# Kernel optimization log

Measured on AMD Instinct MI355X. Metric: run time of the kernel, lower is better.

## Reference

```python
import jax, jax.numpy as jnp
import numpy as np

D_MODEL = 1024
NUM_HEADS = 16
HEAD_DIM = D_MODEL // NUM_HEADS
B, SX, SKV = 4, 2048, 2048


def setup_inputs() -> dict:
    key = jax.random.key(0)
    ks = jax.random.split(key, 6)
    scale = 1.0 / np.sqrt(D_MODEL)
    x = jax.random.normal(ks[0], (B, SX, D_MODEL), dtype=jnp.float32)
    kv = jax.random.normal(ks[1], (B, SKV, D_MODEL), dtype=jnp.float32)
    Wq = jax.random.normal(ks[2], (D_MODEL, D_MODEL), dtype=jnp.float32) * scale
    Wk = jax.random.normal(ks[3], (D_MODEL, D_MODEL), dtype=jnp.float32) * scale
    Wv = jax.random.normal(ks[4], (D_MODEL, D_MODEL), dtype=jnp.float32) * scale
    Wo = jax.random.normal(ks[5], (D_MODEL, D_MODEL), dtype=jnp.float32) * scale
    # causal mask: positions where mask == 0 are filled with -inf
    mask = jnp.tril(jnp.ones((SX, SKV), dtype=jnp.int32))[None, None, :, :]
    return {"x": x, "kv": kv, "mask": mask, "Wq": Wq, "Wk": Wk, "Wv": Wv, "Wo": Wo}


def reference(x, kv, mask, Wq, Wk, Wv, Wo):
    # nn.Linear(bias=False): y = x @ W.T
    q = jnp.einsum('bsd,ed->bse', x, Wq)
    k = jnp.einsum('bsd,ed->bse', kv, Wk)
    v = jnp.einsum('bsd,ed->bse', kv, Wv)
    # split heads -> (B, H, S, hd)
    q = q.reshape(B, SX, NUM_HEADS, HEAD_DIM).transpose(0, 2, 1, 3)
    k = k.reshape(B, SKV, NUM_HEADS, HEAD_DIM).transpose(0, 2, 1, 3)
    v = v.reshape(B, SKV, NUM_HEADS, HEAD_DIM).transpose(0, 2, 1, 3)
    scores = jnp.einsum('bhqd,bhkd->bhqk', q, k) / jnp.sqrt(
        jnp.asarray(HEAD_DIM, dtype=q.dtype))
    scores = jnp.where(mask == 0, -jnp.inf, scores)
    attn = jax.nn.softmax(scores, axis=-1)  # dropout p=0.0 -> identity
    context = jnp.einsum('bhqk,bhkd->bhqd', attn, v)
    context = context.transpose(0, 2, 1, 3).reshape(B, SX, D_MODEL)
    return jnp.einsum('bsd,ed->bse', context, Wo)
```

## Files before the change

### kernel.cpp

```cpp
#include <hip/hip_runtime.h>
#include <hip/hip_bf16.h>
#include <math.h>

#define DM   1024
#define SEQ  2048
#define NH   16
#define HD   64
#define BATCH 4

#define QSCALE 0.180336879f

typedef __attribute__((ext_vector_type(8))) short bf16x8;
typedef __attribute__((ext_vector_type(4))) short short4v;
typedef __attribute__((ext_vector_type(4))) float f32x4;
typedef __attribute__((ext_vector_type(4))) float float4v;

#define S_VMCNT(n) asm volatile("s_waitcnt vmcnt(" #n ")" ::: "memory")

static __device__ inline short f2bf(float f) {
  union { float f; unsigned u; } v; v.f = f;
  unsigned u = v.u + 0x7fff + ((v.u >> 16) & 1);
  return (short)(u >> 16);
}

static __device__ __forceinline__ void async16(const void* g, void* l) {
  __builtin_amdgcn_global_load_lds(
      (const __attribute__((address_space(1))) void*)g,
      (__attribute__((address_space(3))) void*)l, 16, 0, 0);
}

__global__ void conv_all(const float* __restrict__ x, const float* __restrict__ kv,
                         const float* __restrict__ Wq, const float* __restrict__ Wk,
                         const float* __restrict__ Wv, const float* __restrict__ Wo,
                         short* __restrict__ xh, short* __restrict__ kvh,
                         short* __restrict__ Wqh, short* __restrict__ Wkh,
                         short* __restrict__ Wvh, short* __restrict__ Woh)
{
  const int blk = blockIdx.x;
  const float* src; short* hi; int base;
  if (blk < 8192)       { src = x;  hi = xh;  base = blk; }
  else if (blk < 16384) { src = kv; hi = kvh; base = blk - 8192; }
  else {
    int wi = (blk - 16384) >> 10; base = (blk - 16384) & 1023;
    src = wi == 0 ? Wq : wi == 1 ? Wk : wi == 2 ? Wv : Wo;
    hi  = wi == 0 ? Wqh : wi == 1 ? Wkh : wi == 2 ? Wvh : Woh;
  }
  int i = base * 1024 + threadIdx.x * 4;
  float4v v = *(const float4v*)(src + i);
  short4v h;
#pragma unroll
  for (int j = 0; j < 4; j++) h[j] = f2bf(v[j]);
  *(short4v*)(hi + i) = h;
}

static __device__ __forceinline__ void gemm_core(
    const short* __restrict__ A, const short* __restrict__ Bh,
    short* __restrict__ As, short* __restrict__ Bs,
    int m0, int n0, f32x4 acc[4][4])
{
  const int t = threadIdx.x;
  const int lane = t & 63, w = t >> 6;
  const int r15 = lane & 15, quad = lane >> 4;
  const int wm = (w & 1) * 64, wn = (w >> 1) * 64;
  const int srow = t >> 3;
  const int spg = ((t & 7) ^ (srow & 7)) * 8;
  const int swb = (r15 & 7) * 8;
  const int NT = DM / 64;

#pragma unroll
  for (int i = 0; i < 4; i++)
#pragma unroll
    for (int j = 0; j < 4; j++) acc[i][j] = (f32x4)0.0f;

  auto stage = [&](int kt, int bufi) {
    const int k0 = kt * 64;
    short* Ad = As + bufi * 8192 + t * 8;
    short* Bd = Bs + bufi * 8192 + t * 8;
#pragma unroll
    for (int i = 0; i < 4; i++) {
      async16(A  + (size_t)(m0 + srow + 32 * i) * DM + k0 + spg, Ad + i * 2048);
      async16(Bh + (size_t)(n0 + srow + 32 * i) * DM + k0 + spg, Bd + i * 2048);
    }
  };

  stage(0, 0);
  stage(1, 1);

  for (int kt = 0; kt < NT; kt++) {
    const int cur = kt & 1;
    if (kt + 1 < NT) { S_VMCNT(8); } else { S_VMCNT(0); }
    __builtin_amdgcn_s_barrier();
    __builtin_amdgcn_sched_barrier(0);

    const short* Ab = As + cur * 8192;
    const short* Bb = Bs + cur * 8192;
    bf16x8 ah[4][2], bh[4][2];
#pragma unroll
    for (int mt = 0; mt < 4; mt++) {
      const int ro = (wm + mt * 16 + r15) * 64;
#pragma unroll
      for (int ks = 0; ks < 2; ks++)
        ah[mt][ks] = *(const bf16x8*)&Ab[ro + (((ks * 4 + quad) * 8) ^ swb)];
    }
#pragma unroll
    for (int nt = 0; nt < 4; nt++) {
      const int ro = (wn + nt * 16 + r15) * 64;
#pragma unroll
      for (int ks = 0; ks < 2; ks++)
        bh[nt][ks] = *(const bf16x8*)&Bb[ro + (((ks * 4 + quad) * 8) ^ swb)];
    }

    __builtin_amdgcn_s_setprio(1);
#pragma unroll
    for (int mt = 0; mt < 4; mt++)
#pragma unroll
      for (int nt = 0; nt < 4; nt++) {
        acc[mt][nt] = __builtin_amdgcn_mfma_f32_16x16x32_bf16(ah[mt][0], bh[nt][0], acc[mt][nt], 0, 0, 0);
        acc[mt][nt] = __builtin_amdgcn_mfma_f32_16x16x32_bf16(ah[mt][1], bh[nt][1], acc[mt][nt], 0, 0, 0);
      }
    __builtin_amdgcn_s_setprio(0);

    __builtin_amdgcn_s_barrier();
    __builtin_amdgcn_sched_barrier(0);
    if (kt + 2 < NT) stage(kt + 2, cur);
  }
}

__global__ __launch_bounds__(256, 2)
void gemm_qkv(const short* __restrict__ xh, const short* __restrict__ kvh,
              const short* __restrict__ Wqh, const short* __restrict__ Wkh,
              const short* __restrict__ Wvh,
              short* __restrict__ Qh, short* __restrict__ Kh, short* __restrict__ Vt)
{
  __shared__ short As[2][8192];
  __shared__ short Bs[2][8192];
  const int gid = blockIdx.x;
  const int xblk = gid / 192;
  const int rem  = gid - xblk * 192;
  const int yblk = rem / 3;
  const int z    = rem - yblk * 3;
  const short* A  = (z == 0) ? xh : kvh;
  const short* Bm = (z == 0) ? Wqh : (z == 1) ? Wkh : Wvh;
  const int m0 = yblk * 128, n0 = xblk * 128;

  f32x4 acc[4][4];
  gemm_core(A, Bm, &As[0][0], &Bs[0][0], m0, n0, acc);

  const int t = threadIdx.x, lane = t & 63, w = t >> 6;
  const int r15 = lane & 15, quad = lane >> 4;
  const int wm = (w & 1) * 64, wn = (w >> 1) * 64;

  if (z < 2) {
    short* Cp = (z == 0) ? Qh : Kh;
    const float scale = (z == 0) ? QSCALE : 1.0f;
#pragma unroll
    for (int mt = 0; mt < 4; mt++)
#pragma unroll
      for (int nt = 0; nt < 4; nt++)
#pragma unroll
        for (int reg = 0; reg < 4; reg++) {
          int m = m0 + wm + mt * 16 + quad * 4 + reg;
          int n = n0 + wn + nt * 16 + r15;
          Cp[(size_t)m * DM + n] = f2bf(acc[mt][nt][reg] * scale);
        }
  } else {
#pragma unroll
    for (int mt = 0; mt < 4; mt++)
#pragma unroll
      for (int nt = 0; nt < 4; nt++)
#pragma unroll
        for (int reg = 0; reg < 4; reg++) {
          int m = m0 + wm + mt * 16 + quad * 4 + reg;
          int n = n0 + wn + nt * 16 + r15;
          int s = m & (SEQ - 1), kl = s & 63;
          int sp = (s & ~63) + ((kl & 15) * 4 + (kl >> 4));
          Vt[((size_t)(m >> 11) * DM + n) * SEQ + sp] = f2bf(acc[mt][nt][reg]);
        }
  }
}

__global__ __launch_bounds__(256, 2)
void gemm_out(const short* __restrict__ ctx, const short* __restrict__ Woh,
              float* __restrict__ out)
{
  __shared__ short As[2][8192];
  __shared__ short Bs[2][8192];
  const int gid = blockIdx.x;
  const int xblk = gid >> 6;
  const int yblk = gid & 63;
  const int m0 = yblk * 128, n0 = xblk * 128;
  f32x4 acc[4][4];
  gemm_core(ctx, Woh, &As[0][0], &Bs[0][0], m0, n0, acc);

  const int t = threadIdx.x, lane = t & 63, w = t >> 6;
  const int r15 = lane & 15, quad = lane >> 4;
  const int wm = (w & 1) * 64, wn = (w >> 1) * 64;
#pragma unroll
  for (int mt = 0; mt < 4; mt++)
#pragma unroll
    for (int nt = 0; nt < 4; nt++)
#pragma unroll
      for (int reg = 0; reg < 4; reg++) {
        int m = m0 + wm + mt * 16 + quad * 4 + reg;
        int n = n0 + wn + nt * 16 + r15;
        out[(size_t)m * DM + n] = acc[mt][nt][reg];
      }
}

__global__ __launch_bounds__(256, 3)
void attn(const short* __restrict__ Qh_g, const short* __restrict__ Kh_g,
          const short* __restrict__ Vt_g, short* __restrict__ ctx)
{
  __shared__ short KV[2][2 * 4096];
  __shared__ short Plds[4][32][72];

  const int t = threadIdx.x, lane = t & 63, w = t >> 6;
  const int r15 = lane & 15, quad = lane >> 4;
  const int bh = blockIdx.x, b = bh >> 4, h = bh & 15;
  const int qt = 15 - blockIdx.y;
  const int qw = qt * 128 + w * 32;
  const int nkt = 2 * qt + 2;

  const int srow = t >> 3, spg = (t & 7) ^ (srow & 7);
  const int swb = (r15 & 7) * 8;

  const bf16x8 ones = {0x3F80, 0x3F80, 0x3F80, 0x3F80, 0x3F80, 0x3F80, 0x3F80, 0x3F80};

  bf16x8 qh[2][2];
#pragma unroll
  for (int mt = 0; mt < 2; mt++)
#pragma unroll
    for (int ks = 0; ks < 2; ks++)
      qh[mt][ks] = *(const bf16x8*)(Qh_g + (size_t)(b * SEQ + qw + mt * 16 + r15) * DM
                                    + h * HD + ks * 32 + quad * 8);

  f32x4 o[2][4], ol[2];
#pragma unroll
  for (int mt = 0; mt < 2; mt++) {
    ol[mt] = (f32x4)0.0f;
#pragma unroll
    for (int dt = 0; dt < 4; dt++) o[mt][dt] = (f32x4)0.0f;
  }

  auto stage = [&](int kt, int bufi) {
    short* L = &KV[bufi][0];
    size_t kro = (size_t)(b * SEQ + kt * 64 + srow) * DM + h * HD + spg * 8;
    async16(Kh_g + kro,           L + t * 8);
    async16(Kh_g + kro + 32 * DM, L + 2048 + t * 8);
    size_t vro = (size_t)(b * DM + h * HD + srow) * SEQ + kt * 64 + spg * 8;
    async16(Vt_g + vro,            L + 4096 + t * 8);
    async16(Vt_g + vro + 32 * SEQ, L + 6144 + t * 8);
  };

  stage(0, 0);

  for (int kt = 0; kt < nkt; kt++) {
    __syncthreads();
    if (kt + 1 < nkt) stage(kt + 1, (kt + 1) & 1);
    const short* L = &KV[kt & 1][0];
    const int k0 = kt * 64;
    if (k0 > qw + 31) continue;

    f32x4 s[2][4];
#pragma unroll
    for (int nt = 0; nt < 4; nt++) {
      const int kb = k0 + nt * 16;
      if (kb <= qw + 31) {
        const int ro = (nt * 16 + r15) * 64;
        bf16x8 kh0 = *(const bf16x8*)&L[ro + ((quad * 8) ^ swb)];
        bf16x8 kh1 = *(const bf16x8*)&L[ro + (((4 + quad) * 8) ^ swb)];
        f32x4 a1 = (f32x4)0.0f;
        a1 = __builtin_amdgcn_mfma_f32_16x16x32_bf16(qh[1][0], kh0, a1, 0, 0, 0);
        a1 = __builtin_amdgcn_mfma_f32_16x16x32_bf16(qh[1][1], kh1, a1, 0, 0, 0);
        s[1][nt] = a1;
        if (kb <= qw + 15) {
          f32x4 a0 = (f32x4)0.0f;
          a0 = __builtin_amdgcn_mfma_f32_16x16x32_bf16(qh[0][0], kh0, a0, 0, 0, 0);
          a0 = __builtin_amdgcn_mfma_f32_16x16x32_bf16(qh[0][1], kh1, a0, 0, 0, 0);
          s[0][nt] = a0;
        } else {
          s[0][nt] = (f32x4)(-3e38f);
        }
      } else {
        s[0][nt] = (f32x4)(-3e38f);
        s[1][nt] = (f32x4)(-3e38f);
      }
    }

    unsigned up[2][4][2];
    if (k0 + 63 <= qw) {
#pragma unroll
      for (int mt = 0; mt < 2; mt++)
#pragma unroll
        for (int r = 0; r < 4; r++)
#pragma unroll
          for (int nt = 0; nt < 4; nt++) {
            unsigned pu = __float_as_uint(__builtin_amdgcn_exp2f(s[mt][nt][r]));
            if ((nt & 1) == 0) up[mt][r][nt >> 1] = pu >> 16;
            else               up[mt][r][nt >> 1] |= (pu & 0xFFFF0000u);
          }
    } else {
#pragma unroll
      for (int mt = 0; mt < 2; mt++)
#pragma unroll
        for (int r = 0; r < 4; r++) {
          const int qg = qw + mt * 16 + quad * 4 + r;
#pragma unroll
          for (int nt = 0; nt < 4; nt++) {
            float p = __builtin_amdgcn_exp2f(s[mt][nt][r]);
            p = ((k0 + nt * 16 + r15) > qg) ? 0.0f : p;
            unsigned pu = __float_as_uint(p);
            if ((nt & 1) == 0) up[mt][r][nt >> 1] = pu >> 16;
            else               up[mt][r][nt >> 1] |= (pu & 0xFFFF0000u);
          }
        }
    }

#pragma unroll
    for (int mt = 0; mt < 2; mt++)
#pragma unroll
      for (int r = 0; r < 4; r++)
        *(int2*)&Plds[w][mt * 16 + quad * 4 + r][r15 * 4] =
            make_int2((int)up[mt][r][0], (int)up[mt][r][1]);

#pragma unroll
    for (int ks = 0; ks < 2; ks++) {
      bf16x8 pa0 = *(const bf16x8*)&Plds[w][r15][ks * 32 + quad * 8];
      bf16x8 pa1 = *(const bf16x8*)&Plds[w][16 + r15][ks * 32 + quad * 8];
      ol[0] = __builtin_amdgcn_mfma_f32_16x16x32_bf16(pa0, ones, ol[0], 0, 0, 0);
      ol[1] = __builtin_amdgcn_mfma_f32_16x16x32_bf16(pa1, ones, ol[1], 0, 0, 0);
#pragma unroll
      for (int dt = 0; dt < 4; dt++) {
        bf16x8 vb = *(const bf16x8*)&L[4096 + (dt * 16 + r15) * 64 + (((ks * 4 + quad) * 8) ^ swb)];
        o[0][dt] = __builtin_amdgcn_mfma_f32_16x16x32_bf16(pa0, vb, o[0][dt], 0, 0, 0);
        o[1][dt] = __builtin_amdgcn_mfma_f32_16x16x32_bf16(pa1, vb, o[1][dt], 0, 0, 0);
      }
    }
  }

#pragma unroll
  for (int mt = 0; mt < 2; mt++)
#pragma unroll
    for (int r = 0; r < 4; r++) {
      float inv = 1.0f / ol[mt][r];
      int qrow = qw + mt * 16 + quad * 4 + r;
#pragma unroll
      for (int dt = 0; dt < 4; dt++)
        ctx[((size_t)(b * SEQ + qrow)) * DM + h * HD + dt * 16 + r15] =
            f2bf(o[mt][dt][r] * inv);
    }
}

extern "C" void kernel_launch(void* const* d_in, const int* in_sizes, int n_in,
                              void* d_out, int out_size, void* d_ws, size_t ws_size,
                              hipStream_t stream)
{
  const float* x  = (const float*)d_in[0];
  const float* kv = (const float*)d_in[1];
  const float* Wq = (const float*)d_in[3];
  const float* Wk = (const float*)d_in[4];
  const float* Wv = (const float*)d_in[5];
  const float* Wo = (const float*)d_in[6];

  char* ws = (char*)d_ws;
  const size_t SZ  = (size_t)BATCH * SEQ * DM * sizeof(short);
  const size_t WSZ = (size_t)DM * DM * sizeof(short);
  short* xh  = (short*)(ws + 0 * SZ);
  short* kvh = (short*)(ws + 1 * SZ);
  short* Qh  = (short*)(ws + 2 * SZ);
  short* Kh  = (short*)(ws + 3 * SZ);
  short* Vt  = (short*)(ws + 4 * SZ);
  short* ctx = (short*)(ws + 0 * SZ);
  char*  wb  = ws + 5 * SZ;
  short* Wqh = (short*)(wb + 0 * WSZ);
  short* Wkh = (short*)(wb + 1 * WSZ);
  short* Wvh = (short*)(wb + 2 * WSZ);
  short* Woh = (short*)(wb + 3 * WSZ);

  conv_all<<<20480, 256, 0, stream>>>(x, kv, Wq, Wk, Wv, Wo,
                                      xh, kvh, Wqh, Wkh, Wvh, Woh);

  gemm_qkv<<<1536, 256, 0, stream>>>(xh, kvh, Wqh, Wkh, Wvh, Qh, Kh, Vt);

  dim3 ga(NH * BATCH, 16);
  attn<<<ga, 256, 0, stream>>>(Qh, Kh, Vt, ctx);

  gemm_out<<<512, 256, 0, stream>>>(ctx, Woh, (float*)d_out);
}
```

Measured before the change: 269.0 us.

## Replace QKV projection GEMM with 256x256-tile 8-wave ping-pong kernel

Swaps the 128x128-tile, 4-wave QKV projection GEMM for a 256x256-tile kernel with 512 threads and 128 KB of double-buffered LDS. Each k-step is split into four quadrant sub-steps, with async global-to-LDS loads for the next tiles interleaved between MFMA phases and barriers. The goal is more data reuse per LDS byte and better overlap of loads with MFMA work. In exchange it launches 384 blocks instead of 1536, which can leave CUs unevenly loaded, and the larger accumulator set raises register pressure.

```diff
diff --git a/kernel.cpp b/kernel.cpp
--- a/kernel.cpp
+++ b/kernel.cpp
@@ -16,6 +16,8 @@
 typedef __attribute__((ext_vector_type(4))) float float4v;
 
 #define S_VMCNT(n) asm volatile("s_waitcnt vmcnt(" #n ")" ::: "memory")
+#define BARRIER    asm volatile("s_barrier" ::: "memory")
+#define SCHEDB     __builtin_amdgcn_sched_barrier(0)
 
 static __device__ inline short f2bf(float f) {
   union { float f; unsigned u; } v; v.f = f;
@@ -53,6 +55,170 @@
   *(short4v*)(hi + i) = h;
 }
 
+__global__ __launch_bounds__(512, 2)
+void gemm_qkv8(const short* __restrict__ xh, const short* __restrict__ kvh,
+               const short* __restrict__ Wqh, const short* __restrict__ Wkh,
+               const short* __restrict__ Wvh,
+               short* __restrict__ Qh, short* __restrict__ Kh, short* __restrict__ Vt)
+{
+  __shared__ short lds[65536];
+
+  const int gid = blockIdx.x;
+  const int nblk = gid / 96;
+  const int rm   = gid - nblk * 96;
+  const int mblk = rm / 3, z = rm - mblk * 3;
+  const short* Ag = (z == 0) ? xh : kvh;
+  const short* Bw = (z == 0) ? Wqh : (z == 1) ? Wkh : Wvh;
+  const int m0 = mblk * 256, n0 = nblk * 256;
+
+  const int t = threadIdx.x;
+  const int lane = t & 63, w = t >> 6;
+  const int r15 = lane & 15, quad = lane >> 4;
+  const int wr = w >> 2, wc = w & 3;
+  const int srow = t >> 3;
+  const int spg  = ((t & 7) ^ (srow & 7)) * 8;
+  const int swb  = (r15 & 7) * 8;
+  const int NKT  = DM / 64;
+
+  auto stageA = [&](int kt, int mb) {
+    const short* src = Ag + (size_t)(m0 + mb * 64 + srow) * DM + kt * 64 + spg;
+    short* dst = &lds[(kt & 1) * 32768 + mb * 8192 + t * 8];
+    async16(src,            dst);
+    async16(src + 128 * DM, dst + 4096);
+  };
+  auto stageB = [&](int kt, int nb) {
+    const short* src = Bw + (size_t)(n0 + (t >> 8) * 64 + nb * 32 + (srow & 31)) * DM
+                          + kt * 64 + spg;
+    short* dst = &lds[(kt & 1) * 32768 + 16384 + nb * 8192 + t * 8];
+    async16(src,            dst);
+    async16(src + 128 * DM, dst + 4096);
+  };
+
+  f32x4 acc[8][4];
+#pragma unroll
+  for (int i = 0; i < 8; i++)
+#pragma unroll
+    for (int j = 0; j < 4; j++) acc[i][j] = (f32x4)0.0f;
+
+  stageA(0, 0); stageB(0, 0); stageB(0, 1); stageA(0, 1);
+  stageA(1, 0); stageB(1, 0); stageB(1, 1);
+  S_VMCNT(6);
+  BARRIER; SCHEDB;
+
+  bf16x8 a_lo[4][2], a_hi[4][2], b_lo[2][2], b_hi[2][2];
+
+  for (int kt = 0; kt < NKT; kt++) {
+    const int bb = (kt & 1) * 32768;
+
+#pragma unroll
+    for (int mt = 0; mt < 4; mt++)
+#pragma unroll
+      for (int ks = 0; ks < 2; ks++)
+        a_lo[mt][ks] = *(const bf16x8*)&lds[bb + wr * 4096 + (mt * 16 + r15) * 64
+                                           + (((ks * 4 + quad) * 8) ^ swb)];
+#pragma unroll
+    for (int nt = 0; nt < 2; nt++)
+#pragma unroll
+      for (int ks = 0; ks < 2; ks++)
+        b_lo[nt][ks] = *(const bf16x8*)&lds[bb + 16384 + wc * 2048 + (nt * 16 + r15) * 64
+                                            + (((ks * 4 + quad) * 8) ^ swb)];
+    if (kt + 1 < NKT) stageA(kt + 1, 1);
+    BARRIER; SCHEDB;
+    __builtin_amdgcn_s_setprio(1);
+#pragma unroll
+    for (int mt = 0; mt < 4; mt++)
+#pragma unroll
+      for (int nt = 0; nt < 2; nt++) {
+        acc[mt][nt] = __builtin_amdgcn_mfma_f32_16x16x32_bf16(a_lo[mt][0], b_lo[nt][0], acc[mt][nt], 0, 0, 0);
+        acc[mt][nt] = __builtin_amdgcn_mfma_f32_16x16x32_bf16(a_lo[mt][1], b_lo[nt][1], acc[mt][nt], 0, 0, 0);
+      }
+    __builtin_amdgcn_s_setprio(0);
+    SCHEDB; BARRIER; SCHEDB;
+
+#pragma unroll
+    for (int nt = 0; nt < 2; nt++)
+#pragma unroll
+      for (int ks = 0; ks < 2; ks++)
+        b_hi[nt][ks] = *(const bf16x8*)&lds[bb + 16384 + 8192 + wc * 2048 + (nt * 16 + r15) * 64
+                                            + (((ks * 4 + quad) * 8) ^ swb)];
+    if (kt + 2 < NKT) stageA(kt + 2, 0);
+    BARRIER; SCHEDB;
+    __builtin_amdgcn_s_setprio(1);
+#pragma unroll
+    for (int mt = 0; mt < 4; mt++)
+#pragma unroll
+      for (int nt = 0; nt < 2; nt++) {
+        acc[mt][2 + nt] = __builtin_amdgcn_mfma_f32_16x16x32_bf16(a_lo[mt][0], b_hi[nt][0], acc[mt][2 + nt], 0, 0, 0);
+        acc[mt][2 + nt] = __builtin_amdgcn_mfma_f32_16x16x32_bf16(a_lo[mt][1], b_hi[nt][1], acc[mt][2 + nt], 0, 0, 0);
+      }
+    __builtin_amdgcn_s_setprio(0);
+    SCHEDB; BARRIER; SCHEDB;
+
+#pragma unroll
+    for (int mt = 0; mt < 4; mt++)
+#pragma unroll
+      for (int ks = 0; ks < 2; ks++)
+        a_hi[mt][ks] = *(const bf16x8*)&lds[bb + 8192 + wr * 4096 + (mt * 16 + r15) * 64
+                                            + (((ks * 4 + quad) * 8) ^ swb)];
+    if (kt + 2 < NKT) stageB(kt + 2, 0);
+    BARRIER; SCHEDB;
+    __builtin_amdgcn_s_setprio(1);
+#pragma unroll
+    for (int mt = 0; mt < 4; mt++)
+#pragma unroll
+      for (int nt = 0; nt < 2; nt++) {
+        acc[4 + mt][nt] = __builtin_amdgcn_mfma_f32_16x16x32_bf16(a_hi[mt][0], b_lo[nt][0], acc[4 + mt][nt], 0, 0, 0);
+        acc[4 + mt][nt] = __builtin_amdgcn_mfma_f32_16x16x32_bf16(a_hi[mt][1], b_lo[nt][1], acc[4 + mt][nt], 0, 0, 0);
+      }
+    __builtin_amdgcn_s_setprio(0);
+    SCHEDB; BARRIER; SCHEDB;
+
+    if (kt + 2 < NKT) stageB(kt + 2, 1);
+    BARRIER; SCHEDB;
+    __builtin_amdgcn_s_setprio(1);
+#pragma unroll
+    for (int mt = 0; mt < 4; mt++)
+#pragma unroll
+      for (int nt = 0; nt < 2; nt++) {
+        acc[4 + mt][2 + nt] = __builtin_amdgcn_mfma_f32_16x16x32_bf16(a_hi[mt][0], b_hi[nt][0], acc[4 + mt][2 + nt], 0, 0, 0);
+        acc[4 + mt][2 + nt] = __builtin_amdgcn_mfma_f32_16x16x32_bf16(a_hi[mt][1], b_hi[nt][1], acc[4 + mt][2 + nt], 0, 0, 0);
+      }
+    __builtin_amdgcn_s_setprio(0);
+    SCHEDB;
+    if (kt < NKT - 2)       { S_VMCNT(6); }
+    else if (kt == NKT - 2) { S_VMCNT(0); }
+    BARRIER; SCHEDB;
+  }
+
+  if (z < 2) {
+    short* Cp = (z == 0) ? Qh : Kh;
+    const float scale = (z == 0) ? QSCALE : 1.0f;
+#pragma unroll
+    for (int mt = 0; mt < 8; mt++)
+#pragma unroll
+      for (int nt = 0; nt < 4; nt++)
+#pragma unroll
+        for (int reg = 0; reg < 4; reg++) {
+          int m = m0 + wr * 128 + mt * 16 + quad * 4 + reg;
+          int n = n0 + wc * 64 + nt * 16 + r15;
+          Cp[(size_t)m * DM + n] = f2bf(acc[mt][nt][reg] * scale);
+        }
+  } else {
+#pragma unroll
+    for (int mt = 0; mt < 8; mt++)
+#pragma unroll
+      for (int nt = 0; nt < 4; nt++)
+#pragma unroll
+        for (int reg = 0; reg < 4; reg++) {
+          int m = m0 + wr * 128 + mt * 16 + quad * 4 + reg;
+          int n = n0 + wc * 64 + nt * 16 + r15;
+          int s = m & (SEQ - 1), kl = s & 63;
+          int sp = (s & ~63) + ((kl & 15) * 4 + (kl >> 4));
+          Vt[((size_t)(m >> 11) * DM + n) * SEQ + sp] = f2bf(acc[mt][nt][reg]);
+        }
+  }
+}
+
 static __device__ __forceinline__ void gemm_core(
     const short* __restrict__ A, const short* __restrict__ Bh,
     short* __restrict__ As, short* __restrict__ Bs,
@@ -123,59 +289,6 @@
     __builtin_amdgcn_s_barrier();
     __builtin_amdgcn_sched_barrier(0);
     if (kt + 2 < NT) stage(kt + 2, cur);
-  }
-}
-
-__global__ __launch_bounds__(256, 2)
-void gemm_qkv(const short* __restrict__ xh, const short* __restrict__ kvh,
-              const short* __restrict__ Wqh, const short* __restrict__ Wkh,
-              const short* __restrict__ Wvh,
-              short* __restrict__ Qh, short* __restrict__ Kh, short* __restrict__ Vt)
-{
-  __shared__ short As[2][8192];
-  __shared__ short Bs[2][8192];
-  const int gid = blockIdx.x;
-  const int xblk = gid / 192;
-  const int rem  = gid - xblk * 192;
-  const int yblk = rem / 3;
-  const int z    = rem - yblk * 3;
-  const short* A  = (z == 0) ? xh : kvh;
-  const short* Bm = (z == 0) ? Wqh : (z == 1) ? Wkh : Wvh;
-  const int m0 = yblk * 128, n0 = xblk * 128;
-
-  f32x4 acc[4][4];
-  gemm_core(A, Bm, &As[0][0], &Bs[0][0], m0, n0, acc);
-
-  const int t = threadIdx.x, lane = t & 63, w = t >> 6;
-  const int r15 = lane & 15, quad = lane >> 4;
-  const int wm = (w & 1) * 64, wn = (w >> 1) * 64;
-
-  if (z < 2) {
-    short* Cp = (z == 0) ? Qh : Kh;
-    const float scale = (z == 0) ? QSCALE : 1.0f;
-#pragma unroll
-    for (int mt = 0; mt < 4; mt++)
-#pragma unroll
-      for (int nt = 0; nt < 4; nt++)
-#pragma unroll
-        for (int reg = 0; reg < 4; reg++) {
-          int m = m0 + wm + mt * 16 + quad * 4 + reg;
-          int n = n0 + wn + nt * 16 + r15;
-          Cp[(size_t)m * DM + n] = f2bf(acc[mt][nt][reg] * scale);
-        }
-  } else {
-#pragma unroll
-    for (int mt = 0; mt < 4; mt++)
-#pragma unroll
-      for (int nt = 0; nt < 4; nt++)
-#pragma unroll
-        for (int reg = 0; reg < 4; reg++) {
-          int m = m0 + wm + mt * 16 + quad * 4 + reg;
-          int n = n0 + wn + nt * 16 + r15;
-          int s = m & (SEQ - 1), kl = s & 63;
-          int sp = (s & ~63) + ((kl & 15) * 4 + (kl >> 4));
-          Vt[((size_t)(m >> 11) * DM + n) * SEQ + sp] = f2bf(acc[mt][nt][reg]);
-        }
   }
 }
 
@@ -380,7 +493,7 @@
   conv_all<<<20480, 256, 0, stream>>>(x, kv, Wq, Wk, Wv, Wo,
                                       xh, kvh, Wqh, Wkh, Wvh, Woh);
 
-  gemm_qkv<<<1536, 256, 0, stream>>>(xh, kvh, Wqh, Wkh, Wvh, Qh, Kh, Vt);
+  gemm_qkv8<<<384, 512, 0, stream>>>(xh, kvh, Wqh, Wkh, Wvh, Qh, Kh, Vt);
 
   dim3 ga(NH * BATCH, 16);
   attn<<<ga, 256, 0, stream>>>(Qh, Kh, Vt, ctx);
```

Result: no change. 270.1 us (+0.4%).
